# Kernel tuning notes

Hardware: AMD Instinct MI355X
Metric: run time of the kernel (lower is better)

The kernel has to match this reference:

```python
import jax, jax.numpy as jnp
import numpy as np

N_NODES = 100000
N_EDGES = 1600000
NODE_DIM = 5
HIDDEN = 64
N_LAYERS = 3


def setup_inputs() -> dict:
    key = jax.random.key(0)
    ks = jax.random.split(key, 12)
    s = 0.1
    return {
        "x": jax.random.normal(ks[0], (N_NODES, NODE_DIM), dtype=jnp.float32),
        "edge_index": jax.random.randint(ks[1], (2, N_EDGES), 0, N_NODES, dtype=jnp.int32),
        # message MLP params per layer (stacked over layers)
        "W1": jax.random.normal(ks[2], (N_LAYERS, 2 * NODE_DIM, HIDDEN), dtype=jnp.float32) * s,
        "b1": jnp.zeros((N_LAYERS, HIDDEN), dtype=jnp.float32),
        "W2": jax.random.normal(ks[3], (N_LAYERS, HIDDEN, NODE_DIM), dtype=jnp.float32) * s,
        "b2": jnp.zeros((N_LAYERS, NODE_DIM), dtype=jnp.float32),
        # update MLP params per layer
        "U1": jax.random.normal(ks[4], (N_LAYERS, 2 * NODE_DIM, HIDDEN), dtype=jnp.float32) * s,
        "bu1": jnp.zeros((N_LAYERS, HIDDEN), dtype=jnp.float32),
        "U2": jax.random.normal(ks[5], (N_LAYERS, HIDDEN, NODE_DIM), dtype=jnp.float32) * s,
        "bu2": jnp.zeros((N_LAYERS, NODE_DIM), dtype=jnp.float32),
        # readout
        "Wr": jax.random.normal(ks[6], (NODE_DIM, NODE_DIM), dtype=jnp.float32) * s,
        "br": jnp.zeros((NODE_DIM,), dtype=jnp.float32),
    }


def reference(x, edge_index, W1, b1, W2, b2, U1, bu1, U2, bu2, Wr, br):
    # PyG convention: messages flow from source j = edge_index[0] to target i = edge_index[1]
    src = edge_index[0]
    dst = edge_index[1]
    n = x.shape[0]
    for l in range(N_LAYERS):
        x_i = x[dst]                                   # [E, d] target features
        x_j = x[src]                                   # [E, d] source features
        msg_in = jnp.concatenate([x_i, x_j], axis=-1)  # [E, 2d]
        msg = jax.nn.relu(msg_in @ W1[l] + b1[l]) @ W2[l] + b2[l]   # [E, d]
        aggr = jax.ops.segment_sum(msg, dst, num_segments=n)        # [N, d] scatter-add at targets
        upd_in = jnp.concatenate([x, aggr], axis=-1)   # [N, 2d]
        upd = jax.nn.relu(upd_in @ U1[l] + bu1[l]) @ U2[l] + bu2[l]  # [N, d]
        x = upd + x                                    # residual (in SkeletonGNN.forward)
    return x @ Wr + br
```

## Files before the change

### kernel.cpp

```cpp
#include <hip/hip_runtime.h>

#define N_NODES 100000
#define N_EDGES 1600000
#define DIM 5
#define HID 64
#define N_LAYERS 3
#define SCAN_BLK 256
#define NBLK ((N_NODES + SCAN_BLK - 1) / SCAN_BLK)


__global__ __launch_bounds__(256) void hist_kernel(
    const int* __restrict__ ei, int* __restrict__ cnt, int* __restrict__ rank)
{
    int e = blockIdx.x * blockDim.x + threadIdx.x;
    if (e >= N_EDGES) return;
    int dst = ei[N_EDGES + e];
    rank[e] = atomicAdd(&cnt[dst], 1);
}

__global__ __launch_bounds__(SCAN_BLK) void scan_part_kernel(
    const int* __restrict__ cnt, int* __restrict__ blk_sum)
{
    __shared__ int s[SCAN_BLK];
    int t = threadIdx.x;
    int i = blockIdx.x * SCAN_BLK + t;
    s[t] = (i < N_NODES) ? cnt[i] : 0;
    __syncthreads();
    for (int off = SCAN_BLK / 2; off > 0; off >>= 1) {
        if (t < off) s[t] += s[t + off];
        __syncthreads();
    }
    if (t == 0) blk_sum[blockIdx.x] = s[0];
}

__global__ __launch_bounds__(512) void scan_blk_kernel(
    const int* __restrict__ blk_sum, int* __restrict__ blk_pref)
{
    __shared__ int s[512];
    int t = threadIdx.x;
    int v = (t < NBLK) ? blk_sum[t] : 0;
    s[t] = v;
    __syncthreads();
    for (int off = 1; off < 512; off <<= 1) {
        int a = (t >= off) ? s[t - off] : 0;
        __syncthreads();
        s[t] += a;
        __syncthreads();
    }
    if (t < NBLK) blk_pref[t] = s[t] - v;
}

__global__ __launch_bounds__(SCAN_BLK) void scan_add_kernel(
    const int* __restrict__ cnt, const int* __restrict__ blk_pref,
    int* __restrict__ row_ptr)
{
    __shared__ int s[SCAN_BLK];
    int t = threadIdx.x;
    int i = blockIdx.x * SCAN_BLK + t;
    int c = (i < N_NODES) ? cnt[i] : 0;
    s[t] = c;
    __syncthreads();
    for (int off = 1; off < SCAN_BLK; off <<= 1) {
        int a = (t >= off) ? s[t - off] : 0;
        __syncthreads();
        s[t] += a;
        __syncthreads();
    }
    if (i < N_NODES) row_ptr[i] = blk_pref[blockIdx.x] + s[t] - c;
    if (i == 0) row_ptr[N_NODES] = N_EDGES;
}

__global__ __launch_bounds__(256) void scatter_kernel(
    const int* __restrict__ ei, const int* __restrict__ rank,
    const int* __restrict__ row_ptr,
    int* __restrict__ ssrc, int* __restrict__ sdst)
{
    int e = blockIdx.x * blockDim.x + threadIdx.x;
    if (e >= N_EDGES) return;
    int src = ei[e];
    int dst = ei[N_EDGES + e];
    int pos = row_ptr[dst] + rank[e];
    ssrc[pos] = src;
    sdst[pos] = dst;
}


__global__ __launch_bounds__(256) void edge_msg_sorted_kernel(
    const float* __restrict__ x,
    const int* __restrict__ ssrc, const int* __restrict__ sdst,
    const float* __restrict__ W1, const float* __restrict__ b1,
    const float* __restrict__ W2, const float* __restrict__ b2,
    float* __restrict__ msg_buf)
{
    int e = blockIdx.x * blockDim.x + threadIdx.x;
    if (e >= N_EDGES) return;
    int src = ssrc[e];
    int dst = sdst[e];

    float in[10];
    const float* xi = x + (long)dst * DIM;
    const float* xj = x + (long)src * DIM;
#pragma unroll
    for (int d = 0; d < DIM; ++d) in[d] = xi[d];
#pragma unroll
    for (int d = 0; d < DIM; ++d) in[DIM + d] = xj[d];

    float msg[DIM];
#pragma unroll
    for (int j = 0; j < DIM; ++j) msg[j] = b2[j];

#pragma unroll 4
    for (int h = 0; h < HID; ++h) {
        float acc = b1[h];
#pragma unroll
        for (int d = 0; d < 10; ++d) acc = fmaf(in[d], W1[d * HID + h], acc);
        acc = fmaxf(acc, 0.0f);
#pragma unroll
        for (int j = 0; j < DIM; ++j) msg[j] = fmaf(acc, W2[h * DIM + j], msg[j]);
    }

    float* mp = msg_buf + (long)e * DIM;
#pragma unroll
    for (int j = 0; j < DIM; ++j) mp[j] = msg[j];
}

template <bool FINAL>
__global__ __launch_bounds__(256) void node_gather_update_kernel(
    const float* __restrict__ x,
    const float* __restrict__ msg_buf,
    const int* __restrict__ row_ptr,
    const float* __restrict__ U1, const float* __restrict__ bu1,
    const float* __restrict__ U2, const float* __restrict__ bu2,
    const float* __restrict__ Wr, const float* __restrict__ br,
    float* __restrict__ xout)
{
    int v = blockIdx.x * blockDim.x + threadIdx.x;
    if (v >= N_NODES) return;

    float in[10];
#pragma unroll
    for (int d = 0; d < DIM; ++d) in[d] = x[(long)v * DIM + d];

    float agg[DIM] = {0.f, 0.f, 0.f, 0.f, 0.f};
    int s = row_ptr[v], epos = row_ptr[v + 1];
    for (int e = s; e < epos; ++e) {
        const float* mp = msg_buf + (long)e * DIM;
#pragma unroll
        for (int j = 0; j < DIM; ++j) agg[j] += mp[j];
    }
#pragma unroll
    for (int d = 0; d < DIM; ++d) in[DIM + d] = agg[d];

    float upd[DIM];
#pragma unroll
    for (int j = 0; j < DIM; ++j) upd[j] = bu2[j];

#pragma unroll 4
    for (int h = 0; h < HID; ++h) {
        float acc = bu1[h];
#pragma unroll
        for (int d = 0; d < 10; ++d) acc = fmaf(in[d], U1[d * HID + h], acc);
        acc = fmaxf(acc, 0.0f);
#pragma unroll
        for (int j = 0; j < DIM; ++j) upd[j] = fmaf(acc, U2[h * DIM + j], upd[j]);
    }

    float xn[DIM];
#pragma unroll
    for (int j = 0; j < DIM; ++j) xn[j] = upd[j] + in[j];

    if (FINAL) {
#pragma unroll
        for (int j = 0; j < DIM; ++j) {
            float o = br[j];
#pragma unroll
            for (int d = 0; d < DIM; ++d) o = fmaf(xn[d], Wr[d * DIM + j], o);
            xout[(long)v * DIM + j] = o;
        }
    } else {
#pragma unroll
        for (int j = 0; j < DIM; ++j) xout[(long)v * DIM + j] = xn[j];
    }
}


__global__ __launch_bounds__(256) void edge_msg_kernel(
    const float* __restrict__ x, const int* __restrict__ ei,
    const float* __restrict__ W1, const float* __restrict__ b1,
    const float* __restrict__ W2, const float* __restrict__ b2,
    float* __restrict__ aggr)
{
    int e = blockIdx.x * blockDim.x + threadIdx.x;
    if (e >= N_EDGES) return;
    int src = ei[e];
    int dst = ei[N_EDGES + e];
    float in[10];
    const float* xi = x + (long)dst * DIM;
    const float* xj = x + (long)src * DIM;
#pragma unroll
    for (int d = 0; d < DIM; ++d) in[d] = xi[d];
#pragma unroll
    for (int d = 0; d < DIM; ++d) in[DIM + d] = xj[d];
    float msg[DIM];
#pragma unroll
    for (int j = 0; j < DIM; ++j) msg[j] = b2[j];
#pragma unroll 4
    for (int h = 0; h < HID; ++h) {
        float acc = b1[h];
#pragma unroll
        for (int d = 0; d < 10; ++d) acc = fmaf(in[d], W1[d * HID + h], acc);
        acc = fmaxf(acc, 0.0f);
#pragma unroll
        for (int j = 0; j < DIM; ++j) msg[j] = fmaf(acc, W2[h * DIM + j], msg[j]);
    }
    float* ap = aggr + (long)dst * DIM;
#pragma unroll
    for (int j = 0; j < DIM; ++j) atomicAdd(ap + j, msg[j]);
}

template <bool FINAL>
__global__ __launch_bounds__(256) void node_upd_kernel(
    const float* __restrict__ x, const float* __restrict__ aggr,
    const float* __restrict__ U1, const float* __restrict__ bu1,
    const float* __restrict__ U2, const float* __restrict__ bu2,
    const float* __restrict__ Wr, const float* __restrict__ br,
    float* __restrict__ xout)
{
    int v = blockIdx.x * blockDim.x + threadIdx.x;
    if (v >= N_NODES) return;
    float in[10];
#pragma unroll
    for (int d = 0; d < DIM; ++d) in[d] = x[(long)v * DIM + d];
#pragma unroll
    for (int d = 0; d < DIM; ++d) in[DIM + d] = aggr[(long)v * DIM + d];
    float upd[DIM];
#pragma unroll
    for (int j = 0; j < DIM; ++j) upd[j] = bu2[j];
#pragma unroll 4
    for (int h = 0; h < HID; ++h) {
        float acc = bu1[h];
#pragma unroll
        for (int d = 0; d < 10; ++d) acc = fmaf(in[d], U1[d * HID + h], acc);
        acc = fmaxf(acc, 0.0f);
#pragma unroll
        for (int j = 0; j < DIM; ++j) upd[j] = fmaf(acc, U2[h * DIM + j], upd[j]);
    }
    float xn[DIM];
#pragma unroll
    for (int j = 0; j < DIM; ++j) xn[j] = upd[j] + in[j];
    if (FINAL) {
#pragma unroll
        for (int j = 0; j < DIM; ++j) {
            float o = br[j];
#pragma unroll
            for (int d = 0; d < DIM; ++d) o = fmaf(xn[d], Wr[d * DIM + j], o);
            xout[(long)v * DIM + j] = o;
        }
    } else {
#pragma unroll
        for (int j = 0; j < DIM; ++j) xout[(long)v * DIM + j] = xn[j];
    }
}


static inline size_t alignup(size_t x) { return (x + 255) & ~(size_t)255; }

extern "C" void kernel_launch(void* const* d_in, const int* in_sizes, int n_in,
                              void* d_out, int out_size, void* d_ws, size_t ws_size,
                              hipStream_t stream) {
    const float* x   = (const float*)d_in[0];
    const int*   ei  = (const int*)d_in[1];
    const float* W1  = (const float*)d_in[2];
    const float* b1  = (const float*)d_in[3];
    const float* W2  = (const float*)d_in[4];
    const float* b2  = (const float*)d_in[5];
    const float* U1  = (const float*)d_in[6];
    const float* bu1 = (const float*)d_in[7];
    const float* U2  = (const float*)d_in[8];
    const float* bu2 = (const float*)d_in[9];
    const float* Wr  = (const float*)d_in[10];
    const float* br  = (const float*)d_in[11];
    float* out = (float*)d_out;

    char* ws = (char*)d_ws;

    size_t o_cnt  = 0;
    size_t o_row  = alignup(o_cnt + (size_t)N_NODES * 4);
    size_t o_bsum = alignup(o_row + (size_t)(N_NODES + 1) * 4);
    size_t o_bpre = alignup(o_bsum + (size_t)NBLK * 4);
    size_t o_ssrc = alignup(o_bpre + (size_t)NBLK * 4);
    size_t o_sdst = alignup(o_ssrc + (size_t)N_EDGES * 4);
    size_t o_xA   = alignup(o_sdst + (size_t)N_EDGES * 4);
    size_t o_xB   = alignup(o_xA + (size_t)N_NODES * DIM * 4);
    size_t o_msg  = alignup(o_xB + (size_t)N_NODES * DIM * 4);
    size_t needed = o_msg + (size_t)N_EDGES * DIM * 4;

    dim3 blk(256);
    dim3 eg((N_EDGES + 255) / 256);
    dim3 ng((N_NODES + 255) / 256);

    if (ws_size < needed) {
        size_t nbytes = (size_t)N_NODES * DIM * sizeof(float);
        float* aggr = (float*)ws;
        float* xA   = (float*)(ws + nbytes);
        float* xB   = (float*)(ws + 2 * nbytes);
        const float* xcur = x;
        for (int l = 0; l < N_LAYERS; ++l) {
            hipMemsetAsync(aggr, 0, nbytes, stream);
            edge_msg_kernel<<<eg, blk, 0, stream>>>(
                xcur, ei, W1 + l * 10 * HID, b1 + l * HID,
                W2 + l * HID * DIM, b2 + l * DIM, aggr);
            if (l < N_LAYERS - 1) {
                float* xn = (l == 0) ? xA : xB;
                node_upd_kernel<false><<<ng, blk, 0, stream>>>(
                    xcur, aggr, U1 + l * 10 * HID, bu1 + l * HID,
                    U2 + l * HID * DIM, bu2 + l * DIM, Wr, br, xn);
                xcur = xn;
            } else {
                node_upd_kernel<true><<<ng, blk, 0, stream>>>(
                    xcur, aggr, U1 + l * 10 * HID, bu1 + l * HID,
                    U2 + l * HID * DIM, bu2 + l * DIM, Wr, br, out);
            }
        }
        return;
    }

    int* cnt      = (int*)(ws + o_cnt);
    int* row_ptr  = (int*)(ws + o_row);
    int* blk_sum  = (int*)(ws + o_bsum);
    int* blk_pref = (int*)(ws + o_bpre);
    int* ssrc     = (int*)(ws + o_ssrc);
    int* sdst     = (int*)(ws + o_sdst);
    float* xA     = (float*)(ws + o_xA);
    float* xB     = (float*)(ws + o_xB);
    float* msgbuf = (float*)(ws + o_msg);
    int* rank     = (int*)(ws + o_msg);

    hipMemsetAsync(cnt, 0, (size_t)N_NODES * 4, stream);
    hist_kernel<<<eg, blk, 0, stream>>>(ei, cnt, rank);
    scan_part_kernel<<<NBLK, SCAN_BLK, 0, stream>>>(cnt, blk_sum);
    scan_blk_kernel<<<1, 512, 0, stream>>>(blk_sum, blk_pref);
    scan_add_kernel<<<NBLK, SCAN_BLK, 0, stream>>>(cnt, blk_pref, row_ptr);
    scatter_kernel<<<eg, blk, 0, stream>>>(ei, rank, row_ptr, ssrc, sdst);

    const float* xcur = x;
    for (int l = 0; l < N_LAYERS; ++l) {
        edge_msg_sorted_kernel<<<eg, blk, 0, stream>>>(
            xcur, ssrc, sdst, W1 + l * 10 * HID, b1 + l * HID,
            W2 + l * HID * DIM, b2 + l * DIM, msgbuf);
        if (l < N_LAYERS - 1) {
            float* xn = (l == 0) ? xA : xB;
            node_gather_update_kernel<false><<<ng, blk, 0, stream>>>(
                xcur, msgbuf, row_ptr, U1 + l * 10 * HID, bu1 + l * HID,
                U2 + l * HID * DIM, bu2 + l * DIM, Wr, br, xn);
            xcur = xn;
        } else {
            node_gather_update_kernel<true><<<ng, blk, 0, stream>>>(
                xcur, msgbuf, row_ptr, U1 + l * 10 * HID, bu1 + l * HID,
                U2 + l * HID * DIM, bu2 + l * DIM, Wr, br, out);
        }
    }
}
```

Baseline: 410.7 us.

## Fuse edge message MLP into per-node gather-update kernel and pad histogram counters

Computes each node's incoming edge messages inside the node update kernel, looping over the node's CSR edges and accumulating directly into registers. This removes the per-edge message buffer write and read-back plus the sdst array, and folds the b2 bias in once as deg*b2. It also spreads histogram counters to a 16-int stride to reduce atomic contention on the same cache lines. The trade-off is that each thread now does deg×64-hidden MLP work serially, so per-node degree imbalance causes warp divergence and the total parallelism drops from edges to nodes.

```diff
diff --git a/kernel.cpp b/kernel.cpp
--- a/kernel.cpp
+++ b/kernel.cpp
@@ -7,6 +7,7 @@
 #define N_LAYERS 3
 #define SCAN_BLK 256
 #define NBLK ((N_NODES + SCAN_BLK - 1) / SCAN_BLK)
+#define CNT_STRIDE 16
 
 
 __global__ __launch_bounds__(256) void hist_kernel(
@@ -15,7 +16,7 @@
     int e = blockIdx.x * blockDim.x + threadIdx.x;
     if (e >= N_EDGES) return;
     int dst = ei[N_EDGES + e];
-    rank[e] = atomicAdd(&cnt[dst], 1);
+    rank[e] = atomicAdd(&cnt[(long)dst * CNT_STRIDE], 1);
 }
 
 __global__ __launch_bounds__(SCAN_BLK) void scan_part_kernel(
@@ -24,7 +25,7 @@
     __shared__ int s[SCAN_BLK];
     int t = threadIdx.x;
     int i = blockIdx.x * SCAN_BLK + t;
-    s[t] = (i < N_NODES) ? cnt[i] : 0;
+    s[t] = (i < N_NODES) ? cnt[(long)i * CNT_STRIDE] : 0;
     __syncthreads();
     for (int off = SCAN_BLK / 2; off > 0; off >>= 1) {
         if (t < off) s[t] += s[t + off];
@@ -57,7 +58,7 @@
     __shared__ int s[SCAN_BLK];
     int t = threadIdx.x;
     int i = blockIdx.x * SCAN_BLK + t;
-    int c = (i < N_NODES) ? cnt[i] : 0;
+    int c = (i < N_NODES) ? cnt[(long)i * CNT_STRIDE] : 0;
     s[t] = c;
     __syncthreads();
     for (int off = 1; off < SCAN_BLK; off <<= 1) {
@@ -70,65 +71,24 @@
     if (i == 0) row_ptr[N_NODES] = N_EDGES;
 }
 
-__global__ __launch_bounds__(256) void scatter_kernel(
+__global__ __launch_bounds__(256) void scatter_src_kernel(
     const int* __restrict__ ei, const int* __restrict__ rank,
-    const int* __restrict__ row_ptr,
-    int* __restrict__ ssrc, int* __restrict__ sdst)
+    const int* __restrict__ row_ptr, int* __restrict__ ssrc)
 {
     int e = blockIdx.x * blockDim.x + threadIdx.x;
     if (e >= N_EDGES) return;
     int src = ei[e];
     int dst = ei[N_EDGES + e];
-    int pos = row_ptr[dst] + rank[e];
-    ssrc[pos] = src;
-    sdst[pos] = dst;
-}
-
-
-__global__ __launch_bounds__(256) void edge_msg_sorted_kernel(
+    ssrc[row_ptr[dst] + rank[e]] = src;
+}
+
+template <bool FINAL>
+__global__ __launch_bounds__(256) void fused_layer_kernel(
     const float* __restrict__ x,
-    const int* __restrict__ ssrc, const int* __restrict__ sdst,
+    const int* __restrict__ ssrc,
+    const int* __restrict__ row_ptr,
     const float* __restrict__ W1, const float* __restrict__ b1,
     const float* __restrict__ W2, const float* __restrict__ b2,
-    float* __restrict__ msg_buf)
-{
-    int e = blockIdx.x * blockDim.x + threadIdx.x;
-    if (e >= N_EDGES) return;
-    int src = ssrc[e];
-    int dst = sdst[e];
-
-    float in[10];
-    const float* xi = x + (long)dst * DIM;
-    const float* xj = x + (long)src * DIM;
-#pragma unroll
-    for (int d = 0; d < DIM; ++d) in[d] = xi[d];
-#pragma unroll
-    for (int d = 0; d < DIM; ++d) in[DIM + d] = xj[d];
-
-    float msg[DIM];
-#pragma unroll
-    for (int j = 0; j < DIM; ++j) msg[j] = b2[j];
-
-#pragma unroll 4
-    for (int h = 0; h < HID; ++h) {
-        float acc = b1[h];
-#pragma unroll
-        for (int d = 0; d < 10; ++d) acc = fmaf(in[d], W1[d * HID + h], acc);
-        acc = fmaxf(acc, 0.0f);
-#pragma unroll
-        for (int j = 0; j < DIM; ++j) msg[j] = fmaf(acc, W2[h * DIM + j], msg[j]);
-    }
-
-    float* mp = msg_buf + (long)e * DIM;
-#pragma unroll
-    for (int j = 0; j < DIM; ++j) mp[j] = msg[j];
-}
-
-template <bool FINAL>
-__global__ __launch_bounds__(256) void node_gather_update_kernel(
-    const float* __restrict__ x,
-    const float* __restrict__ msg_buf,
-    const int* __restrict__ row_ptr,
     const float* __restrict__ U1, const float* __restrict__ bu1,
     const float* __restrict__ U2, const float* __restrict__ bu2,
     const float* __restrict__ Wr, const float* __restrict__ br,
@@ -137,19 +97,42 @@
     int v = blockIdx.x * blockDim.x + threadIdx.x;
     if (v >= N_NODES) return;
 
-    float in[10];
-#pragma unroll
-    for (int d = 0; d < DIM; ++d) in[d] = x[(long)v * DIM + d];
+    float xv[DIM];
+#pragma unroll
+    for (int d = 0; d < DIM; ++d) xv[d] = x[(long)v * DIM + d];
+
+    int s = row_ptr[v], epos = row_ptr[v + 1];
+    int deg = epos - s;
 
     float agg[DIM] = {0.f, 0.f, 0.f, 0.f, 0.f};
-    int s = row_ptr[v], epos = row_ptr[v + 1];
     for (int e = s; e < epos; ++e) {
-        const float* mp = msg_buf + (long)e * DIM;
-#pragma unroll
-        for (int j = 0; j < DIM; ++j) agg[j] += mp[j];
-    }
-#pragma unroll
-    for (int d = 0; d < DIM; ++d) in[DIM + d] = agg[d];
+        int src = ssrc[e];
+        float in[10];
+#pragma unroll
+        for (int d = 0; d < DIM; ++d) in[d] = xv[d];
+        const float* xs = x + (long)src * DIM;
+#pragma unroll
+        for (int d = 0; d < DIM; ++d) in[DIM + d] = xs[d];
+
+#pragma unroll 4
+        for (int h = 0; h < HID; ++h) {
+            float acc = b1[h];
+#pragma unroll
+            for (int d = 0; d < 10; ++d) acc = fmaf(in[d], W1[d * HID + h], acc);
+            acc = fmaxf(acc, 0.0f);
+#pragma unroll
+            for (int j = 0; j < DIM; ++j) agg[j] = fmaf(acc, W2[h * DIM + j], agg[j]);
+        }
+    }
+    float degf = (float)deg;
+#pragma unroll
+    for (int j = 0; j < DIM; ++j) agg[j] = fmaf(degf, b2[j], agg[j]);
+
+    float in2[10];
+#pragma unroll
+    for (int d = 0; d < DIM; ++d) in2[d] = xv[d];
+#pragma unroll
+    for (int d = 0; d < DIM; ++d) in2[DIM + d] = agg[d];
 
     float upd[DIM];
 #pragma unroll
@@ -159,7 +142,7 @@
     for (int h = 0; h < HID; ++h) {
         float acc = bu1[h];
 #pragma unroll
-        for (int d = 0; d < 10; ++d) acc = fmaf(in[d], U1[d * HID + h], acc);
+        for (int d = 0; d < 10; ++d) acc = fmaf(in2[d], U1[d * HID + h], acc);
         acc = fmaxf(acc, 0.0f);
 #pragma unroll
         for (int j = 0; j < DIM; ++j) upd[j] = fmaf(acc, U2[h * DIM + j], upd[j]);
@@ -167,7 +150,7 @@
 
     float xn[DIM];
 #pragma unroll
-    for (int j = 0; j < DIM; ++j) xn[j] = upd[j] + in[j];
+    for (int j = 0; j < DIM; ++j) xn[j] = upd[j] + xv[j];
 
     if (FINAL) {
 #pragma unroll
@@ -285,15 +268,14 @@
     char* ws = (char*)d_ws;
 
     size_t o_cnt  = 0;
-    size_t o_row  = alignup(o_cnt + (size_t)N_NODES * 4);
+    size_t o_row  = alignup(o_cnt + (size_t)N_NODES * CNT_STRIDE * 4);
     size_t o_bsum = alignup(o_row + (size_t)(N_NODES + 1) * 4);
     size_t o_bpre = alignup(o_bsum + (size_t)NBLK * 4);
     size_t o_ssrc = alignup(o_bpre + (size_t)NBLK * 4);
-    size_t o_sdst = alignup(o_ssrc + (size_t)N_EDGES * 4);
-    size_t o_xA   = alignup(o_sdst + (size_t)N_EDGES * 4);
+    size_t o_rank = alignup(o_ssrc + (size_t)N_EDGES * 4);
+    size_t o_xA   = alignup(o_rank + (size_t)N_EDGES * 4);
     size_t o_xB   = alignup(o_xA + (size_t)N_NODES * DIM * 4);
-    size_t o_msg  = alignup(o_xB + (size_t)N_NODES * DIM * 4);
-    size_t needed = o_msg + (size_t)N_EDGES * DIM * 4;
+    size_t needed = alignup(o_xB + (size_t)N_NODES * DIM * 4);
 
     dim3 blk(256);
     dim3 eg((N_EDGES + 255) / 256);
@@ -330,34 +312,37 @@
     int* blk_sum  = (int*)(ws + o_bsum);
     int* blk_pref = (int*)(ws + o_bpre);
     int* ssrc     = (int*)(ws + o_ssrc);
-    int* sdst     = (int*)(ws + o_sdst);
+    int* rank     = (int*)(ws + o_rank);
     float* xA     = (float*)(ws + o_xA);
     float* xB     = (float*)(ws + o_xB);
-    float* msgbuf = (float*)(ws + o_msg);
-    int* rank     = (int*)(ws + o_msg);
-
-    hipMemsetAsync(cnt, 0, (size_t)N_NODES * 4, stream);
+
+    hipMemsetAsync(cnt, 0, (size_t)N_NODES * CNT_STRIDE * 4, stream);
     hist_kernel<<<eg, blk, 0, stream>>>(ei, cnt, rank);
     scan_part_kernel<<<NBLK, SCAN_BLK, 0, stream>>>(cnt, blk_sum);
     scan_blk_kernel<<<1, 512, 0, stream>>>(blk_sum, blk_pref);
     scan_add_kernel<<<NBLK, SCAN_BLK, 0, stream>>>(cnt, blk_pref, row_ptr);
-    scatter_kernel<<<eg, blk, 0, stream>>>(ei, rank, row_ptr, ssrc, sdst);
+    scatter_src_kernel<<<eg, blk, 0, stream>>>(ei, rank, row_ptr, ssrc);
 
     const float* xcur = x;
     for (int l = 0; l < N_LAYERS; ++l) {
-        edge_msg_sorted_kernel<<<eg, blk, 0, stream>>>(
-            xcur, ssrc, sdst, W1 + l * 10 * HID, b1 + l * HID,
-            W2 + l * HID * DIM, b2 + l * DIM, msgbuf);
+        const float* W1l = W1 + l * 10 * HID;
+        const float* b1l = b1 + l * HID;
+        const float* W2l = W2 + l * HID * DIM;
+        const float* b2l = b2 + l * DIM;
+        const float* U1l = U1 + l * 10 * HID;
+        const float* bu1l = bu1 + l * HID;
+        const float* U2l = U2 + l * HID * DIM;
+        const float* bu2l = bu2 + l * DIM;
         if (l < N_LAYERS - 1) {
             float* xn = (l == 0) ? xA : xB;
-            node_gather_update_kernel<false><<<ng, blk, 0, stream>>>(
-                xcur, msgbuf, row_ptr, U1 + l * 10 * HID, bu1 + l * HID,
-                U2 + l * HID * DIM, bu2 + l * DIM, Wr, br, xn);
+            fused_layer_kernel<false><<<ng, blk, 0, stream>>>(
+                xcur, ssrc, row_ptr, W1l, b1l, W2l, b2l,
+                U1l, bu1l, U2l, bu2l, Wr, br, xn);
             xcur = xn;
         } else {
-            node_gather_update_kernel<true><<<ng, blk, 0, stream>>>(
-                xcur, msgbuf, row_ptr, U1 + l * 10 * HID, bu1 + l * HID,
-                U2 + l * HID * DIM, bu2 + l * DIM, Wr, br, out);
-        }
-    }
-}
+            fused_layer_kernel<true><<<ng, blk, 0, stream>>>(
+                xcur, ssrc, row_ptr, W1l, b1l, W2l, b2l,
+                U1l, bu1l, U2l, bu2l, Wr, br, out);
+        }
+    }
+}
```

Result: slower. 674.2 us (+64.2%).
